# Kernel tuning notes

Hardware: AMD Instinct MI355X
Metric: run time of the kernel (lower is better)

Reference implementation:

```python
import jax, jax.numpy as jnp
import numpy as np

H = 2048          # hidden size
N_HEADS = 16
HEAD_DIM = H // N_HEADS   # 128
ATTN_SCALE = 8.0          # attention_scale > 1.0 -> custom max-subtract path
B, S = 2, 2048


def setup_inputs() -> dict:
    key = jax.random.key(0)
    k1, k2, k3, k4, k5 = jax.random.split(key, 5)
    hidden_states = jax.random.normal(k1, (B, S, H), dtype=jnp.float32)
    # causal left-to-right multiplicative mask, broadcast over batch and heads
    ltor_mask = jnp.tril(jnp.ones((S, S), dtype=jnp.float32))[None, None]
    std = 0.02
    W_qkv = jax.random.normal(k2, (H, 3 * H), dtype=jnp.float32) * std
    b_qkv = jnp.zeros((3 * H,), dtype=jnp.float32)
    W_out = jax.random.normal(k3, (H, H), dtype=jnp.float32) * std
    b_out = jnp.zeros((H,), dtype=jnp.float32)
    return {"hidden_states": hidden_states, "ltor_mask": ltor_mask,
            "W_qkv": W_qkv, "b_qkv": b_qkv, "W_out": W_out, "b_out": b_out}


def reference(hidden_states, ltor_mask, W_qkv, b_qkv, W_out, b_out):
    b, s, h = hidden_states.shape
    # fused QKV projection: [b, s, 3h]
    qkv = jnp.einsum('bsh,hk->bsk', hidden_states, W_qkv) + b_qkv
    q, k, v = jnp.split(qkv, 3, axis=-1)
    # [b, s, h] -> [b, n, s, hn]
    def to_heads(t):
        return t.reshape(b, s, N_HEADS, HEAD_DIM).transpose(0, 2, 1, 3)
    q, k, v = to_heads(q), to_heads(k), to_heads(v)
    # custom scale: q / sqrt(scale), k / sqrt(hn * scale)
    inv = 1.0 / (ATTN_SCALE * np.sqrt(np.float32(HEAD_DIM)))
    scores = jnp.einsum('bnqd,bnkd->bnqk', q, k) * jnp.float32(inv)
    # multiplicative mask BEFORE max-subtract (zeroes masked positions)
    scores = scores * ltor_mask
    # attention_scale > 1.0 path: subtract row max, re-multiply by scale
    scores = (scores - jnp.max(scores, axis=-1, keepdims=True)) * jnp.float32(ATTN_SCALE)
    # additive large-negative fill on masked entries
    scores = scores + jnp.float32(-65504.0) * (1.0 - ltor_mask)
    probs = jax.nn.softmax(scores, axis=-1)
    ctx = jnp.einsum('bnqk,bnkd->bnqd', probs, v)
    ctx = ctx.transpose(0, 2, 1, 3).reshape(b, s, h)
    out = jnp.einsum('bsh,hk->bsk', ctx, W_out) + b_out
    return out
```

## Files before the change

kernel.cpp:

```cpp
#include <hip/hip_runtime.h>

#define S_LEN 2048
#define HDIM  2048
#define NHEADS 16
#define DHEAD 128
#define BATCH 2
#define MROWS (BATCH * S_LEN)
#define QKVN  (3 * HDIM)

typedef _Float16 f16;
typedef _Float16 f16x8 __attribute__((ext_vector_type(8)));
typedef _Float16 f16x4 __attribute__((ext_vector_type(4)));
typedef float    f32x4 __attribute__((ext_vector_type(4)));
typedef float    f32x16 __attribute__((ext_vector_type(16)));

typedef const __attribute__((address_space(1))) void* gas_ptr;
typedef __attribute__((address_space(3))) void*       las_ptr;

#define MFMA16(a, b, c)  __builtin_amdgcn_mfma_f32_16x16x32_f16(a, b, c, 0, 0, 0)
#define MFMA32(a, b, c)  __builtin_amdgcn_mfma_f32_32x32x16_f16(a, b, c, 0, 0, 0)

__device__ __forceinline__ void gl_lds16(const f16* g, f16* lds_wave_base) {
#if defined(__has_builtin) && __has_builtin(__builtin_amdgcn_global_load_lds)
  __builtin_amdgcn_global_load_lds((gas_ptr)g, (las_ptr)lds_wave_base, 16, 0, 0);
#else
  int lane = threadIdx.x & 63;
  ((f16x8*)lds_wave_base)[lane] = *(const f16x8*)g;
#endif
}


__device__ __forceinline__ void transpose_tile(const float* __restrict__ W,
                                               f16* __restrict__ Wb,
                                               int K, int N, int k0, int n0,
                                               float* tile ) {
  int tr = threadIdx.x >> 4;
  int tc = (threadIdx.x & 15) * 4;
  int KT = K >> 5;
#pragma unroll
  for (int rr = 0; rr < 4; ++rr) {
    int r = rr * 16 + tr;
    float4 v = *(const float4*)(W + (size_t)(k0 + r) * N + n0 + tc);
    tile[r * 65 + tc + 0] = v.x; tile[r * 65 + tc + 1] = v.y;
    tile[r * 65 + tc + 2] = v.z; tile[r * 65 + tc + 3] = v.w;
  }
  __syncthreads();
#pragma unroll
  for (int rr = 0; rr < 4; ++rr) {
    int r = rr * 16 + tr;
    int n = n0 + r;
    int kBase = k0 + tc;
    f16x4 o;
#pragma unroll
    for (int c = 0; c < 4; ++c) o[c] = (f16)tile[(tc + c) * 65 + r];
    int nt = n >> 7, nn = n & 127;
    int kt = kBase >> 5, kc = (kBase >> 3) & 3, j = kBase & 7;
    *(f16x4*)(Wb + ((size_t)nt * KT + kt) * 4096 + (kc * 128 + nn) * 8 + j) = o;
  }
}

__global__ __launch_bounds__(256) void prep_kernel(const float* __restrict__ X,
                                                   f16* __restrict__ Xb,
                                                   const float* __restrict__ Wqkv,
                                                   f16* __restrict__ Wqkvb,
                                                   const float* __restrict__ Wout,
                                                   f16* __restrict__ Woutb) {
  __shared__ float tile[64 * 65];
  int bz = blockIdx.x;
  if (bz < 2048) {
    int kt = bz & 63, rt = bz >> 6;
    int t = threadIdx.x;
    int m = t >> 1, half = t & 1;
    const float* src = X + (size_t)(rt * 128 + m) * HDIM + kt * 32 + half * 16;
    float4 v0 = ((const float4*)src)[0];
    float4 v1 = ((const float4*)src)[1];
    float4 v2 = ((const float4*)src)[2];
    float4 v3 = ((const float4*)src)[3];
    f16x8 a = {(f16)v0.x, (f16)v0.y, (f16)v0.z, (f16)v0.w,
               (f16)v1.x, (f16)v1.y, (f16)v1.z, (f16)v1.w};
    f16x8 b = {(f16)v2.x, (f16)v2.y, (f16)v2.z, (f16)v2.w,
               (f16)v3.x, (f16)v3.y, (f16)v3.z, (f16)v3.w};
    f16* dst = Xb + ((size_t)rt * 64 + kt) * 4096 + ((half * 2) * 128 + m) * 8;
    *(f16x8*)dst = a;
    *(f16x8*)(dst + 1024) = b;
  } else if (bz < 5120) {
    int u = bz - 2048;
    int nx = u % 96, ky = u / 96;
    transpose_tile(Wqkv, Wqkvb, HDIM, QKVN, ky * 64, nx * 64, tile);
  } else {
    int u = bz - 5120;
    int nx = u & 31, ky = u >> 5;
    transpose_tile(Wout, Woutb, HDIM, HDIM, ky * 64, nx * 64, tile);
  }
}

template <int MODE>
__global__ __launch_bounds__(256) void gemm_kernel(const f16* __restrict__ Ablk,
                                                   const f16* __restrict__ Bblk,
                                                   const float* __restrict__ bias,
                                                   f16* __restrict__ Cpart,
                                                   f16* __restrict__ Qr,
                                                   f16* __restrict__ KB,
                                                   f16* __restrict__ VB,
                                                   int moff, int M, int N, int K) {
  __shared__ f16 As[4 * 128 * 8];
  __shared__ f16 Bs[4 * 128 * 8];
  int tid = threadIdx.x;
  int lane = tid & 63, w = tid >> 6;
  int lhi = lane >> 4, llo = lane & 15;
  int by = moff + blockIdx.y;
  int m0 = by * 128, n0 = blockIdx.x * 128;
  int wm = (w & 1) * 64, wn = (w >> 1) * 64;
  int KT = K >> 5;
  const f16* Ab = Ablk + (size_t)by * KT * 4096;
  const f16* Bb = Bblk + (size_t)blockIdx.x * KT * 4096;

  int ktBeg = 0, ktEnd = KT;
  if (MODE == 2) { int half = KT >> 1; ktBeg = blockIdx.z * half; ktEnd = ktBeg + half; }

  f32x4 acc[4][4];
#pragma unroll
  for (int i = 0; i < 4; ++i)
#pragma unroll
    for (int j = 0; j < 4; ++j) acc[i][j] = (f32x4){0.f, 0.f, 0.f, 0.f};

  for (int kt = ktBeg; kt < ktEnd; ++kt) {
    __syncthreads();
#pragma unroll
    for (int i2 = 0; i2 < 2; ++i2) {
      int Lw = i2 * 256 + w * 64;
      gl_lds16(Ab + (size_t)kt * 4096 + Lw * 8 + (lane * 8), As + Lw * 8);
      gl_lds16(Bb + (size_t)kt * 4096 + Lw * 8 + (lane * 8), Bs + Lw * 8);
    }
    __syncthreads();

    f16x8 af[4], bf[4];
#pragma unroll
    for (int i = 0; i < 4; ++i)
      af[i] = *(const f16x8*)(As + (lhi * 128 + wm + i * 16 + llo) * 8);
#pragma unroll
    for (int j = 0; j < 4; ++j)
      bf[j] = *(const f16x8*)(Bs + (lhi * 128 + wn + j * 16 + llo) * 8);
#pragma unroll
    for (int i = 0; i < 4; ++i)
#pragma unroll
      for (int j = 0; j < 4; ++j) acc[i][j] = MFMA16(af[i], bf[j], acc[i][j]);
  }

#pragma unroll
  for (int j = 0; j < 4; ++j) {
    int col = n0 + wn + j * 16 + llo;
    float bv = (MODE == 1) ? bias[col] : 0.f;
#pragma unroll
    for (int i = 0; i < 4; ++i) {
      int rowb = m0 + wm + i * 16 + lhi * 4;
      if (MODE == 2) {
        size_t zoff = (size_t)blockIdx.z * M * N;
#pragma unroll
        for (int r = 0; r < 4; ++r)
          Cpart[zoff + (size_t)(rowb + r) * N + col] = (f16)acc[i][j][r];
      } else {
        int region = n0 >> 11;
        if (region == 0) {
#pragma unroll
          for (int r = 0; r < 4; ++r)
            Qr[(size_t)(rowb + r) * HDIM + col] = (f16)(acc[i][j][r] + bv);
        } else if (region == 1) {
          int cK = col - HDIM;
          int hd = cK >> 7, d = cK & 127, g = d >> 3, dj = d & 7;
#pragma unroll
          for (int r = 0; r < 4; ++r) {
            int row = rowb + r;
            int b = row >> 11, s = row & 2047;
            int kt2 = s >> 6, key = s & 63;
            size_t addr = ((((size_t)(b * 16 + hd) * 32 + kt2) * 16 + g) * 64 + key) * 8 + dj;
            KB[addr] = (f16)(acc[i][j][r] + bv);
          }
        } else {
          int cV = col - 2 * HDIM;
          int hd = cV >> 7, d = cV & 127;
          int row = rowb;
          int b = row >> 11, s = row & 2047;
          int kt2 = s >> 6, key = s & 63;
          int kg = key >> 3, kj = key & 7;
          f16x4 pv = {(f16)(acc[i][j][0] + bv), (f16)(acc[i][j][1] + bv),
                      (f16)(acc[i][j][2] + bv), (f16)(acc[i][j][3] + bv)};
          size_t addr = ((((size_t)(b * 16 + hd) * 32 + kt2) * 8 + kg) * 128 + d) * 8 + kj;
          *(f16x4*)(VB + addr) = pv;
        }
      }
    }
  }
}

__global__ __launch_bounds__(256) void merge_out_kernel(const f16* __restrict__ Cpart,
                                                        const float* __restrict__ bias,
                                                        float* __restrict__ out) {
  int t = blockIdx.x * 256 + threadIdx.x;
  int col8 = (t & 255) * 8;
  int row = t >> 8;
  size_t base = (size_t)row * HDIM + col8;
  const size_t MN = (size_t)MROWS * HDIM;
  f16x8 a = *(const f16x8*)(Cpart + base);
  f16x8 b = *(const f16x8*)(Cpart + MN + base);
  float4 b0 = *(const float4*)(bias + col8);
  float4 b1 = *(const float4*)(bias + col8 + 4);
  float4 o0 = {(float)a[0] + (float)b[0] + b0.x, (float)a[1] + (float)b[1] + b0.y,
               (float)a[2] + (float)b[2] + b0.z, (float)a[3] + (float)b[3] + b0.w};
  float4 o1 = {(float)a[4] + (float)b[4] + b1.x, (float)a[5] + (float)b[5] + b1.y,
               (float)a[6] + (float)b[6] + b1.z, (float)a[7] + (float)b[7] + b1.w};
  *(float4*)(out + base) = o0;
  *(float4*)(out + base + 4) = o1;
}

__global__ __launch_bounds__(256, 3) void attn_kernel(const f16* __restrict__ Qr,
                                                      const f16* __restrict__ KB,
                                                      const f16* __restrict__ VB,
                                                      f16* __restrict__ Opart,
                                                      float* __restrict__ Lpart) {
  __shared__ f16 Ks[1024 * 8];
  __shared__ f16 Vs[1024 * 8];
  __shared__ f16 Ps[4][32 * 72];

  int tid = threadIdx.x, lane = tid & 63, w = tid >> 6;
  int l5 = lane & 31, hl = lane >> 5;
  int bh = blockIdx.y, b = bh >> 4, hd = bh & 15;
  int gx = blockIdx.x;
  int qt, kt0, kt1, slot;
  if (gx < 8) { qt = gx; slot = 0; kt0 = 0; kt1 = 2 * qt + 2; }
  else {
    qt = 8 + ((gx - 8) >> 1); slot = (gx - 8) & 1;
    kt0 = slot ? (qt + 1) : 0;
    kt1 = slot ? (2 * qt + 2) : (qt + 1);
  }

  int qbase = qt * 128 + w * 32;
  int qrow = qbase + l5;

  const f16* qp = Qr + (size_t)(b * S_LEN + qrow) * HDIM + hd * DHEAD + hl * 8;
  f16x8 qf[8];
#pragma unroll
  for (int s8 = 0; s8 < 8; ++s8) qf[s8] = *(const f16x8*)(qp + s8 * 16);

  f32x16 oac[4];
#pragma unroll
  for (int mt = 0; mt < 4; ++mt)
#pragma unroll
    for (int r = 0; r < 16; ++r) oac[mt][r] = 0.f;
  float rs = 0.f;

  const float C1 = 0.12752747419986393f;
  const float C2 = 11.541560327111708f;

  const f16* KBb = KB + (size_t)bh * 32 * 8192;
  const f16* VBb = VB + (size_t)bh * 32 * 8192;

  for (int kt = kt0; kt < kt1; ++kt) {
    __syncthreads();
    {
      const f16* Kt = KBb + (size_t)kt * 8192;
      const f16* Vt = VBb + (size_t)kt * 8192;
#pragma unroll
      for (int c = 0; c < 4; ++c) {
        int u0 = w * 256 + c * 64;
        gl_lds16(Kt + (size_t)(u0 + lane) * 8, Ks + u0 * 8);
        gl_lds16(Vt + (size_t)(u0 + lane) * 8, Vs + u0 * 8);
      }
    }
    __syncthreads();

    if (kt * 64 <= qbase + 31) {
      f32x16 sac[2];
#pragma unroll
      for (int mt = 0; mt < 2; ++mt)
#pragma unroll
        for (int r = 0; r < 16; ++r) sac[mt][r] = 0.f;
#pragma unroll
      for (int s8 = 0; s8 < 8; ++s8) {
#pragma unroll
        for (int mt = 0; mt < 2; ++mt) {
          f16x8 kf = *(const f16x8*)(Ks + ((s8 * 2 + hl) * 64 + mt * 32 + l5) * 8);
          sac[mt] = MFMA32(kf, qf[s8], sac[mt]);
        }
      }

      bool diag = (kt * 64 + 63 > qbase);
#pragma unroll
      for (int mt = 0; mt < 2; ++mt) {
#pragma unroll
        for (int g4 = 0; g4 < 4; ++g4) {
          f16x4 pk;
#pragma unroll
          for (int r = 0; r < 4; ++r) {
            int keyl = mt * 32 + g4 * 8 + hl * 4 + r;
            float p = __builtin_amdgcn_exp2f(fmaf(sac[mt][g4 * 4 + r], C1, -C2));
            if (diag && (kt * 64 + keyl > qrow)) p = 0.f;
            rs += p;
            pk[r] = (f16)p;
          }
          *(f16x4*)(&Ps[w][l5 * 72 + mt * 32 + g4 * 8 + hl * 4]) = pk;
        }
      }
      asm volatile("s_waitcnt lgkmcnt(0)" ::: "memory");

#pragma unroll
      for (int ks = 0; ks < 4; ++ks) {
        f16x8 pf = *(const f16x8*)(&Ps[w][l5 * 72 + ks * 16 + hl * 8]);
#pragma unroll
        for (int mt = 0; mt < 4; ++mt) {
          f16x8 vf = *(const f16x8*)(Vs + ((ks * 2 + hl) * 128 + mt * 32 + l5) * 8);
          oac[mt] = MFMA32(vf, pf, oac[mt]);
        }
      }
    }
  }

  float lsum = rs + __shfl_xor(rs, 32, 64);
  size_t ob = ((size_t)slot * 32 + bh) * S_LEN * DHEAD + (size_t)qrow * DHEAD;
#pragma unroll
  for (int mt = 0; mt < 4; ++mt) {
#pragma unroll
    for (int g4 = 0; g4 < 4; ++g4) {
      int d = mt * 32 + g4 * 8 + hl * 4;
      f16x4 ov = {(f16)oac[mt][g4 * 4 + 0], (f16)oac[mt][g4 * 4 + 1],
                  (f16)oac[mt][g4 * 4 + 2], (f16)oac[mt][g4 * 4 + 3]};
      *(f16x4*)(Opart + ob + d) = ov;
    }
  }
  if (hl == 0) Lpart[((size_t)slot * 32 + bh) * S_LEN + qrow] = lsum;
}

__global__ __launch_bounds__(256) void merge_kernel(const f16* __restrict__ Opart,
                                                    const float* __restrict__ Lpart,
                                                    f16* __restrict__ CTXb) {
  int t = blockIdx.x * 256 + threadIdx.x;
  int d8 = (t & 15) * 8;
  int q = (t >> 4) & 2047;
  int bh = t >> 15;
  int b = bh >> 4, hd = bh & 15;
  int ns = ((q >> 7) >= 8) ? 2 : 1;
  size_t o0 = ((size_t)bh * S_LEN + q) * DHEAD + d8;
  const size_t OSLOT = (size_t)32 * S_LEN * DHEAD;
  float l = Lpart[(size_t)bh * S_LEN + q];
  f16x8 a = *(const f16x8*)(Opart + o0);
  float acc[8];
#pragma unroll
  for (int j = 0; j < 8; ++j) acc[j] = (float)a[j];
  if (ns == 2) {
    l += Lpart[OSLOT / DHEAD + (size_t)bh * S_LEN + q];
    f16x8 a2 = *(const f16x8*)(Opart + OSLOT + o0);
#pragma unroll
    for (int j = 0; j < 8; ++j) acc[j] += (float)a2[j];
  }
  float inv = 1.0f / l;
  f16x8 o;
#pragma unroll
  for (int j = 0; j < 8; ++j) o[j] = (f16)(acc[j] * inv);
  int row = b * S_LEN + q;
  int col = hd * DHEAD + d8;
  int rt = row >> 7, rr = row & 127;
  int kt = col >> 5, kc = (col >> 3) & 3;
  *(f16x8*)(CTXb + ((size_t)rt * 64 + kt) * 4096 + (kc * 128 + rr) * 8) = o;
}

extern "C" void kernel_launch(void* const* d_in, const int* in_sizes, int n_in,
                              void* d_out, int out_size, void* d_ws, size_t ws_size,
                              hipStream_t stream) {
  const float* X    = (const float*)d_in[0];
  const float* Wqkv = (const float*)d_in[2];
  const float* bqkv = (const float*)d_in[3];
  const float* Wout = (const float*)d_in[4];
  const float* bout = (const float*)d_in[5];
  float* out = (float*)d_out;

  char* ws = (char*)d_ws;
  f16* Xb    = (f16*)ws;  ws += (size_t)MROWS * HDIM * sizeof(f16);
  f16* Wqkvb = (f16*)ws;  ws += (size_t)QKVN * HDIM * sizeof(f16);
  f16* Woutb = (f16*)ws;  ws += (size_t)HDIM * HDIM * sizeof(f16);
  f16* Qr    = (f16*)ws;  ws += (size_t)MROWS * HDIM * sizeof(f16);
  f16* KB    = (f16*)ws;  ws += (size_t)32 * 32 * 8192 * sizeof(f16);
  f16* VB    = (f16*)ws;  ws += (size_t)32 * 32 * 8192 * sizeof(f16);
  f16* Opart = (f16*)ws;  ws += (size_t)2 * 32 * S_LEN * DHEAD * sizeof(f16);
  float* Lpart = (float*)ws;  ws += (size_t)2 * 32 * S_LEN * sizeof(float);
  f16* CTXb  = Xb;
  f16* Cpart = Opart;

  prep_kernel<<<6144, 256, 0, stream>>>(X, Xb, Wqkv, Wqkvb, Wout, Woutb);

  gemm_kernel<1><<<dim3(QKVN / 128, 16), 256, 0, stream>>>(
      Xb, Wqkvb, bqkv, nullptr, Qr, KB, VB, 0, MROWS, QKVN, HDIM);
  gemm_kernel<1><<<dim3(QKVN / 128, 16), 256, 0, stream>>>(
      Xb, Wqkvb, bqkv, nullptr, Qr, KB, VB, 16, MROWS, QKVN, HDIM);

  attn_kernel<<<dim3(24, 32), 256, 0, stream>>>(Qr, KB, VB, Opart, Lpart);

  merge_kernel<<<(32 * S_LEN * 16) / 256, 256, 0, stream>>>(Opart, Lpart, CTXb);

  gemm_kernel<2><<<dim3(HDIM / 128, 32, 2), 256, 0, stream>>>(
      CTXb, Woutb, nullptr, Cpart, nullptr, nullptr, nullptr, 0, MROWS, HDIM, HDIM);

  merge_out_kernel<<<(MROWS * HDIM / 8) / 256, 256, 0, stream>>>(Cpart, bout, out);
}
```

Measured before the change: 408.5 us.

## Enlarge attention query tile to 256 rows with variable split-K segments

The attention kernel now uses 512-thread blocks (8 waves) covering 256 query rows, so each K/V tile loaded into LDS is shared by twice as many query rows. Later query tiles split their causal key range into 1 to 4 segments to balance work across 16 blocks per head, and the merge kernel sums a variable number of partial outputs. This halves K/V load traffic per query row. In exchange the block count drops from 768 to 512, occupancy per CU changes, and later tiles need a wider merge.

```diff
diff --git a/kernel.cpp b/kernel.cpp
--- a/kernel.cpp
+++ b/kernel.cpp
@@ -213,28 +213,30 @@
   *(float4*)(out + base + 4) = o1;
 }
 
-__global__ __launch_bounds__(256, 3) void attn_kernel(const f16* __restrict__ Qr,
+__global__ __launch_bounds__(512, 2) void attn_kernel(const f16* __restrict__ Qr,
                                                       const f16* __restrict__ KB,
                                                       const f16* __restrict__ VB,
                                                       f16* __restrict__ Opart,
                                                       float* __restrict__ Lpart) {
   __shared__ f16 Ks[1024 * 8];
   __shared__ f16 Vs[1024 * 8];
-  __shared__ f16 Ps[4][32 * 72];
+  __shared__ f16 Ps[8][32 * 72];
 
   int tid = threadIdx.x, lane = tid & 63, w = tid >> 6;
   int l5 = lane & 31, hl = lane >> 5;
   int bh = blockIdx.y, b = bh >> 4, hd = bh & 15;
   int gx = blockIdx.x;
-  int qt, kt0, kt1, slot;
-  if (gx < 8) { qt = gx; slot = 0; kt0 = 0; kt1 = 2 * qt + 2; }
-  else {
-    qt = 8 + ((gx - 8) >> 1); slot = (gx - 8) & 1;
-    kt0 = slot ? (qt + 1) : 0;
-    kt1 = slot ? (2 * qt + 2) : (qt + 1);
-  }
-
-  int qbase = qt * 128 + w * 32;
+
+  int qt2, seg, nseg;
+  if (gx < 3)       { qt2 = gx;                 seg = 0;          nseg = 1; }
+  else if (gx < 9)  { int r = gx - 3; qt2 = 3 + (r >> 1); seg = r & 1; nseg = 2; }
+  else if (gx < 12) { qt2 = 6; seg = gx - 9;  nseg = 3; }
+  else              { qt2 = 7; seg = gx - 12; nseg = 4; }
+  int cnt = 4 * qt2 + 4;
+  int kt0 = seg * cnt / nseg;
+  int kt1 = (seg + 1) * cnt / nseg;
+
+  int qbase = qt2 * 256 + w * 32;
   int qrow = qbase + l5;
 
   const f16* qp = Qr + (size_t)(b * S_LEN + qrow) * HDIM + hd * DHEAD + hl * 8;
@@ -261,8 +263,8 @@
       const f16* Kt = KBb + (size_t)kt * 8192;
       const f16* Vt = VBb + (size_t)kt * 8192;
 #pragma unroll
-      for (int c = 0; c < 4; ++c) {
-        int u0 = w * 256 + c * 64;
+      for (int c = 0; c < 2; ++c) {
+        int u0 = w * 128 + c * 64;
         gl_lds16(Kt + (size_t)(u0 + lane) * 8, Ks + u0 * 8);
         gl_lds16(Vt + (size_t)(u0 + lane) * 8, Vs + u0 * 8);
       }
@@ -316,7 +318,9 @@
   }
 
   float lsum = rs + __shfl_xor(rs, 32, 64);
-  size_t ob = ((size_t)slot * 32 + bh) * S_LEN * DHEAD + (size_t)qrow * DHEAD;
+  int lq = w * 32 + l5;
+  size_t slot = (size_t)bh * 16 + gx;
+  size_t ob = slot * (256 * DHEAD) + (size_t)lq * DHEAD;
 #pragma unroll
   for (int mt = 0; mt < 4; ++mt) {
 #pragma unroll
@@ -327,7 +331,7 @@
       *(f16x4*)(Opart + ob + d) = ov;
     }
   }
-  if (hl == 0) Lpart[((size_t)slot * 32 + bh) * S_LEN + qrow] = lsum;
+  if (hl == 0) Lpart[slot * 256 + lq] = lsum;
 }
 
 __global__ __launch_bounds__(256) void merge_kernel(const f16* __restrict__ Opart,
@@ -338,19 +342,19 @@
   int q = (t >> 4) & 2047;
   int bh = t >> 15;
   int b = bh >> 4, hd = bh & 15;
-  int ns = ((q >> 7) >= 8) ? 2 : 1;
-  size_t o0 = ((size_t)bh * S_LEN + q) * DHEAD + d8;
-  const size_t OSLOT = (size_t)32 * S_LEN * DHEAD;
-  float l = Lpart[(size_t)bh * S_LEN + q];
-  f16x8 a = *(const f16x8*)(Opart + o0);
+  int qt2 = q >> 8, lq = q & 255;
+  int nseg = (qt2 < 3) ? 1 : ((qt2 < 6) ? 2 : ((qt2 == 6) ? 3 : 4));
+  int gxbase = (qt2 < 3) ? qt2 : ((qt2 < 6) ? (3 + 2 * (qt2 - 3)) : ((qt2 == 6) ? 9 : 12));
+  size_t slot0 = (size_t)bh * 16 + gxbase;
   float acc[8];
 #pragma unroll
-  for (int j = 0; j < 8; ++j) acc[j] = (float)a[j];
-  if (ns == 2) {
-    l += Lpart[OSLOT / DHEAD + (size_t)bh * S_LEN + q];
-    f16x8 a2 = *(const f16x8*)(Opart + OSLOT + o0);
-#pragma unroll
-    for (int j = 0; j < 8; ++j) acc[j] += (float)a2[j];
+  for (int j = 0; j < 8; ++j) acc[j] = 0.f;
+  float l = 0.f;
+  for (int s = 0; s < nseg; ++s) {
+    l += Lpart[(slot0 + s) * 256 + lq];
+    f16x8 a = *(const f16x8*)(Opart + (slot0 + s) * (256 * DHEAD) + (size_t)lq * DHEAD + d8);
+#pragma unroll
+    for (int j = 0; j < 8; ++j) acc[j] += (float)a[j];
   }
   float inv = 1.0f / l;
   f16x8 o;
@@ -380,8 +384,8 @@
   f16* Qr    = (f16*)ws;  ws += (size_t)MROWS * HDIM * sizeof(f16);
   f16* KB    = (f16*)ws;  ws += (size_t)32 * 32 * 8192 * sizeof(f16);
   f16* VB    = (f16*)ws;  ws += (size_t)32 * 32 * 8192 * sizeof(f16);
-  f16* Opart = (f16*)ws;  ws += (size_t)2 * 32 * S_LEN * DHEAD * sizeof(f16);
-  float* Lpart = (float*)ws;  ws += (size_t)2 * 32 * S_LEN * sizeof(float);
+  f16* Opart = (f16*)ws;  ws += (size_t)32 * 16 * 256 * DHEAD * sizeof(f16);
+  float* Lpart = (float*)ws;  ws += (size_t)32 * 16 * 256 * sizeof(float);
   f16* CTXb  = Xb;
   f16* Cpart = Opart;
 
@@ -392,7 +396,7 @@
   gemm_kernel<1><<<dim3(QKVN / 128, 16), 256, 0, stream>>>(
       Xb, Wqkvb, bqkv, nullptr, Qr, KB, VB, 16, MROWS, QKVN, HDIM);
 
-  attn_kernel<<<dim3(24, 32), 256, 0, stream>>>(Qr, KB, VB, Opart, Lpart);
+  attn_kernel<<<dim3(16, 32), 512, 0, stream>>>(Qr, KB, VB, Opart, Lpart);
 
   merge_kernel<<<(32 * S_LEN * 16) / 256, 256, 0, stream>>>(Opart, Lpart, CTXb);
 
```

Result: slower. 433.5 us (+6.1%).
